# Optimization experiments

Hardware: AMD Instinct MI355X
Metric: run time of the kernel (lower is better)

Reference implementation:

```python
import jax, jax.numpy as jnp
import numpy as np

DIM = 2048
N_HEADS = 16
Q_LORA = 1536
KV_LORA = 512
NOPE = 128
ROPE = 64
QK_HD = NOPE + ROPE  # 192
V_HD = 128
BS, SEQ = 2, 2048
EPS = 1e-6


def rmsnorm(x, w):
    var = jnp.mean(jnp.square(x), axis=-1, keepdims=True)
    return x * jax.lax.rsqrt(var + EPS) * w


def rope_cos_sin(seq_len, dim, dtype):
    inv_freq = 1.0 / (10000.0 ** (jnp.arange(0, dim, 2, dtype=jnp.float32) / dim))
    t = jnp.arange(seq_len, dtype=jnp.float32)
    freqs = jnp.outer(t, inv_freq)            # [S, dim/2]
    emb = jnp.concatenate([freqs, freqs], -1)  # [S, dim]
    return jnp.cos(emb).astype(dtype), jnp.sin(emb).astype(dtype)


def rotate_half(x):
    x1, x2 = jnp.split(x, 2, axis=-1)
    return jnp.concatenate([-x2, x1], axis=-1)


def apply_rope(x, cos, sin):
    # x: [B, S, H, D]; cos/sin: [S, D] -> broadcast over B, H
    return x * cos[None, :, None, :] + rotate_half(x) * sin[None, :, None, :]


def setup_inputs() -> dict:
    key = jax.random.key(0)
    ks = jax.random.split(key, 8)
    s = 0.02
    return {
        "x": jax.random.normal(ks[0], (BS, SEQ, DIM), jnp.float32),
        "wq_a_w": jax.random.normal(ks[1], (Q_LORA, DIM), jnp.float32) * s,
        "wq_a_b": jnp.zeros((Q_LORA,), jnp.float32),
        "q_norm_w": jnp.ones((Q_LORA,), jnp.float32),
        "wq_b_w": jax.random.normal(ks[2], (N_HEADS * QK_HD, Q_LORA), jnp.float32) * s,
        "wq_b_b": jnp.zeros((N_HEADS * QK_HD,), jnp.float32),
        "wkv_a_w": jax.random.normal(ks[3], (KV_LORA + ROPE, DIM), jnp.float32) * s,
        "wkv_a_b": jnp.zeros((KV_LORA + ROPE,), jnp.float32),
        "kv_norm_w": jnp.ones((KV_LORA,), jnp.float32),
        "wkv_b_w": jax.random.normal(ks[4], (N_HEADS * (NOPE + V_HD), KV_LORA), jnp.float32) * s,
        "wkv_b_b": jnp.zeros((N_HEADS * (NOPE + V_HD),), jnp.float32),
        "wo_w": jax.random.normal(ks[5], (DIM, N_HEADS * V_HD), jnp.float32) * s,
        "wo_b": jnp.zeros((DIM,), jnp.float32),
    }


def reference(x, wq_a_w, wq_a_b, q_norm_w, wq_b_w, wq_b_b,
              wkv_a_w, wkv_a_b, kv_norm_w, wkv_b_w, wkv_b_b, wo_w, wo_b):
    bs, seq_len, _ = x.shape
    # Q path: low-rank down, RMSNorm, up
    q = x @ wq_a_w.T + wq_a_b
    q = rmsnorm(q, q_norm_w)
    q = q @ wq_b_w.T + wq_b_b
    q = q.reshape(bs, seq_len, N_HEADS, QK_HD)
    q_nope, q_pe = q[..., :NOPE], q[..., NOPE:]
    # KV path: joint low-rank + decoupled rope key
    kv = x @ wkv_a_w.T + wkv_a_b
    kv_c, k_pe = kv[..., :KV_LORA], kv[..., KV_LORA:]
    k_pe = k_pe[:, :, None, :]  # [B, S, 1, ROPE]
    cos, sin = rope_cos_sin(seq_len, ROPE, x.dtype)
    q_pe = apply_rope(q_pe, cos, sin)
    k_pe = apply_rope(k_pe, cos, sin)
    # naive mode: materialize per-head K/V
    kv_c = rmsnorm(kv_c, kv_norm_w)
    kvb = (kv_c @ wkv_b_w.T + wkv_b_b).reshape(bs, seq_len, N_HEADS, NOPE + V_HD)
    k_nope, v = kvb[..., :NOPE], kvb[..., NOPE:]
    q_full = jnp.concatenate([q_nope, q_pe], axis=-1)            # [B,S,H,192]
    k_full = jnp.concatenate(
        [k_nope, jnp.broadcast_to(k_pe, (bs, seq_len, N_HEADS, ROPE))], axis=-1)
    scale = 1.0 / np.sqrt(QK_HD)
    scores = jnp.einsum('bqhd,bkhd->bhqk', q_full, k_full) * scale
    causal = jnp.tril(jnp.ones((seq_len, seq_len), bool))
    scores = jnp.where(causal[None, None], scores, jnp.finfo(scores.dtype).min)
    attn = jax.nn.softmax(scores, axis=-1)
    out = jnp.einsum('bhqk,bkhd->bqhd', attn, v)
    out = out.reshape(bs, seq_len, N_HEADS * V_HD)
    return out @ wo_w.T + wo_b
```

## Files before the change

kernel.cpp:

```cpp
#include <hip/hip_runtime.h>

#define SEQ 2048
#define NHEADS 16

typedef __bf16 bf16;
typedef __bf16 bf16x8 __attribute__((ext_vector_type(8)));
typedef __bf16 bf16x4v __attribute__((ext_vector_type(4)));
typedef float f32x4 __attribute__((ext_vector_type(4)));

static __device__ __forceinline__ float bf2f(unsigned short u) {
    union { unsigned u32; float f; } v; v.u32 = ((unsigned)u) << 16; return v.f;
}
static __device__ __forceinline__ unsigned short f2bf(float f) {
    union { float f; unsigned u; } v; v.f = f;
    unsigned u = v.u;
    unsigned r = u + 0x7fffu + ((u >> 16) & 1u);
    return (unsigned short)(r >> 16);
}

static __device__ __forceinline__ void g2l16(const unsigned short* g, unsigned short* l) {
    __builtin_amdgcn_global_load_lds(
        (const __attribute__((address_space(1))) unsigned int*)(unsigned long long)g,
        (__attribute__((address_space(3))) unsigned int*)(unsigned int)(unsigned long long)l,
        16, 0, 0);
}

__global__ void detect_dtype(const unsigned* __restrict__ qnw, int* __restrict__ flag) {
    if (threadIdx.x == 0 && blockIdx.x == 0)
        *flag = (qnw[0] == 0x3F800000u) ? 1 : 0;
}

struct CvtArgs {
    const void* src[13];
    unsigned short* dst[13];
    int n[13];
    int startblk[14];
};
__global__ __launch_bounds__(256) void to_bf16_all(CvtArgs a, const int* __restrict__ flag) {
    int bx = blockIdx.x;
    int t = 0;
    while (bx >= a.startblk[t + 1]) ++t;
    int base = (bx - a.startblk[t]) * 4096;
    int n = a.n[t];
    int hi = base + 4096; if (hi > n) hi = n;
    if (*flag) {
        const float* s = (const float*)a.src[t];
        unsigned short* d = a.dst[t];
        for (int e = base + threadIdx.x; e < hi; e += 256) d[e] = f2bf(s[e]);
    } else {
        const unsigned short* s = (const unsigned short*)a.src[t];
        unsigned short* d = a.dst[t];
        for (int e = base + threadIdx.x; e < hi; e += 256) d[e] = s[e];
    }
}

__global__ __launch_bounds__(256) void gemm_bt_tile(
    const unsigned short* __restrict__ A, int lda,
    const unsigned short* __restrict__ W,
    const unsigned short* __restrict__ bias,
    unsigned short* __restrict__ C, float* __restrict__ Cf, int ldc,
    int N, int K, const int* __restrict__ flagp)
{
    __shared__ unsigned short Al[128 * 32];
    __shared__ unsigned short Bl[128 * 32];

    const int lane = threadIdx.x & 63;
    const int w    = threadIdx.x >> 6;
    const int r    = lane & 15;
    const int quad = lane >> 4;
    const int m0 = blockIdx.y << 7;
    const int n0 = blockIdx.x << 7;
    const int wr = (w >> 1) << 6;
    const int wc = (w & 1) << 6;

    const int srow = lane >> 2;
    const int scol = (lane & 3) << 3;
    const int j0 = w * 2, j1 = w * 2 + 1;

    const unsigned short* a0 = A + (size_t)(m0 + j0 * 16 + srow) * lda + scol;
    const unsigned short* a1 = A + (size_t)(m0 + j1 * 16 + srow) * lda + scol;
    int bn0 = n0 + j0 * 16 + srow; if (bn0 >= N) bn0 = N - 1;
    int bn1 = n0 + j1 * 16 + srow; if (bn1 >= N) bn1 = N - 1;
    const unsigned short* b0 = W + (size_t)bn0 * K + scol;
    const unsigned short* b1 = W + (size_t)bn1 * K + scol;

    f32x4 acc[4][4];
#pragma unroll
    for (int mt = 0; mt < 4; ++mt)
#pragma unroll
        for (int nt = 0; nt < 4; ++nt) acc[mt][nt] = (f32x4){0.f, 0.f, 0.f, 0.f};

    for (int kb = 0; kb < K; kb += 32) {
        __syncthreads();
        g2l16(a0 + kb, &Al[j0 * 512 + lane * 8]);
        g2l16(a1 + kb, &Al[j1 * 512 + lane * 8]);
        g2l16(b0 + kb, &Bl[j0 * 512 + lane * 8]);
        g2l16(b1 + kb, &Bl[j1 * 512 + lane * 8]);
        __syncthreads();

        bf16x8 af[4], bfr[4];
#pragma unroll
        for (int mt = 0; mt < 4; ++mt)
            af[mt] = *(const bf16x8*)&Al[(wr + mt * 16 + r) * 32 + quad * 8];
#pragma unroll
        for (int nt = 0; nt < 4; ++nt)
            bfr[nt] = *(const bf16x8*)&Bl[(wc + nt * 16 + r) * 32 + quad * 8];
#pragma unroll
        for (int mt = 0; mt < 4; ++mt)
#pragma unroll
            for (int nt = 0; nt < 4; ++nt)
                acc[mt][nt] = __builtin_amdgcn_mfma_f32_16x16x32_bf16(af[mt], bfr[nt], acc[mt][nt], 0, 0, 0);
    }

    int outf = (Cf && flagp) ? *flagp : 0;
    float bv[4];
#pragma unroll
    for (int nt = 0; nt < 4; ++nt) {
        int col = n0 + wc + nt * 16 + r;
        bv[nt] = (bias && col < N) ? bf2f(bias[col]) : 0.f;
    }
#pragma unroll
    for (int mt = 0; mt < 4; ++mt) {
#pragma unroll
        for (int i = 0; i < 4; ++i) {
            int row = m0 + wr + mt * 16 + quad * 4 + i;
#pragma unroll
            for (int nt = 0; nt < 4; ++nt) {
                int col = n0 + wc + nt * 16 + r;
                if (col < N) {
                    float v = acc[mt][nt][i] + bv[nt];
                    size_t idx = (size_t)row * ldc + col;
                    if (Cf) {
                        if (outf) Cf[idx] = v;
                        else      ((unsigned short*)Cf)[idx] = f2bf(v);
                    } else {
                        C[idx] = f2bf(v);
                    }
                }
            }
        }
    }
}

__global__ __launch_bounds__(256) void rmsnorm_ip(
    unsigned short* __restrict__ data, int stride, int width,
    const unsigned short* __restrict__ w)
{
    __shared__ float red[256];
    int row = blockIdx.x;
    unsigned short* p = data + (size_t)row * stride;
    float ss = 0.f;
    for (int j = threadIdx.x; j < width; j += 256) {
        float f = bf2f(p[j]);
        ss += f * f;
    }
    red[threadIdx.x] = ss;
    __syncthreads();
    for (int s = 128; s > 0; s >>= 1) {
        if ((int)threadIdx.x < s) red[threadIdx.x] += red[threadIdx.x + s];
        __syncthreads();
    }
    float rstd = rsqrtf(red[0] / (float)width + 1e-6f);
    for (int j = threadIdx.x; j < width; j += 256) {
        p[j] = f2bf(bf2f(p[j]) * rstd * bf2f(w[j]));
    }
}

__global__ void rope_ip(unsigned short* __restrict__ base, int rowstride,
                        int headstride, int nheads, int off)
{
    int row = blockIdx.x;
    int s = row & (SEQ - 1);
    int total = nheads * 32;
    for (int t = threadIdx.x; t < total; t += blockDim.x) {
        int h = t >> 5, i = t & 31;
        float inv = exp2f(-(float)i * (13.2877123795f / 32.0f));
        float ang = (float)s * inv;
        float c = cosf(ang), sn = sinf(ang);
        unsigned short* p = base + (size_t)row * rowstride + h * headstride + off;
        float x1 = bf2f(p[i]), x2 = bf2f(p[i + 32]);
        p[i]      = f2bf(x1 * c - x2 * sn);
        p[i + 32] = f2bf(x2 * c + x1 * sn);
    }
}

__global__ __launch_bounds__(256) void mla_attn_mfma(
    const unsigned short* __restrict__ qbuf,
    const unsigned short* __restrict__ kvb,
    const unsigned short* __restrict__ kvbuf,
    unsigned short* __restrict__ attn_out)
{
    __shared__ unsigned short Kt[2][32 * 200];
    __shared__ unsigned short Vt[2][128 * 40];
    __shared__ unsigned short Pm[4][16 * 40];

    const int bh = blockIdx.y;
    const int b = bh >> 4, h = bh & 15;
    const int tid  = threadIdx.x;
    const int lane = tid & 63;
    const int w    = tid >> 6;
    const int r    = lane & 15;
    const int quad = lane >> 4;
    const int rowk0 = b * SEQ;
    const float scale = 0.0721687836487f;

    int kldso[3];
    const unsigned short* ksrc[3];
    int krst[3];
#pragma unroll
    for (int j = 0; j < 3; ++j) {
        int v = tid + j * 256;
        int row = v / 24, c = v % 24;
        kldso[j] = row * 200 + c * 8;
        if (c < 16) { ksrc[j] = kvb + (size_t)(rowk0 + row) * 4096 + h * 256 + c * 8; krst[j] = 4096; }
        else        { ksrc[j] = kvbuf + (size_t)(rowk0 + row) * 576 + 512 + (c - 16) * 8; krst[j] = 576; }
    }
    const int vp  = tid & 15;
    const int vdc = tid >> 4;
    const unsigned short* vsrc = kvb + (size_t)(rowk0 + 2 * vp) * 4096 + h * 256 + 128 + vdc * 8;

    unsigned short* Pw = Pm[w];

#pragma unroll 1
    for (int half = 0; half < 2; ++half) {
        const int qt = half ? (31 - (int)blockIdx.x) : (int)blockIdx.x;
        const int qbase = qt * 64 + w * 16;
        const int nkb = 2 * qt + 2;
        const int itmax = 2 * qt + (w >> 1);

        bf16x8 qf[6];
        {
            const unsigned short* qp =
                qbuf + (size_t)(rowk0 + qbase + r) * 3072 + h * 192 + quad * 8;
#pragma unroll
            for (int t = 0; t < 6; ++t) {
                bf16x8 v = *(const bf16x8*)(qp + t * 32);
#pragma unroll
                for (int j = 0; j < 8; ++j) v[j] = (__bf16)((float)v[j] * scale);
                qf[t] = v;
            }
        }

        f32x4 O[8];
#pragma unroll
        for (int f = 0; f < 8; ++f) O[f] = (f32x4){0.f, 0.f, 0.f, 0.f};
        float mi = -1e30f, li = 0.f;

        uint4 pk0, pk1, pk2, pv0, pv1;

        __syncthreads();
        pk0 = *(const uint4*)(ksrc[0]);
        pk1 = *(const uint4*)(ksrc[1]);
        pk2 = *(const uint4*)(ksrc[2]);
        pv0 = *(const uint4*)(vsrc);
        pv1 = *(const uint4*)(vsrc + 4096);
        {
            *(uint4*)&Kt[0][kldso[0]] = pk0;
            *(uint4*)&Kt[0][kldso[1]] = pk1;
            *(uint4*)&Kt[0][kldso[2]] = pk2;
            const unsigned* ea = (const unsigned*)&pv0;
            const unsigned* eb = (const unsigned*)&pv1;
#pragma unroll
            for (int t = 0; t < 4; ++t) {
                unsigned pe = (ea[t] & 0xffffu) | (eb[t] << 16);
                unsigned po = (ea[t] >> 16) | (eb[t] & 0xffff0000u);
                *(unsigned*)&Vt[0][(vdc * 8 + 2 * t) * 40 + 2 * vp]     = pe;
                *(unsigned*)&Vt[0][(vdc * 8 + 2 * t + 1) * 40 + 2 * vp] = po;
            }
        }
        __syncthreads();

#pragma unroll 1
        for (int it = 0; it < nkb; ++it) {
            const int p = it & 1;
            const int kb = it * 32;
            const bool more = (it + 1 < nkb);

            if (more) {
                const size_t koff = (size_t)(kb + 32);
                pk0 = *(const uint4*)(ksrc[0] + koff * krst[0]);
                pk1 = *(const uint4*)(ksrc[1] + koff * krst[1]);
                pk2 = *(const uint4*)(ksrc[2] + koff * krst[2]);
                pv0 = *(const uint4*)(vsrc + koff * 4096);
                pv1 = *(const uint4*)(vsrc + koff * 4096 + 4096);
            }

            if (it <= itmax) {
                f32x4 s0 = {0.f, 0.f, 0.f, 0.f}, s1 = {0.f, 0.f, 0.f, 0.f};
#pragma unroll
                for (int t = 0; t < 6; ++t) {
                    bf16x8 k0 = *(const bf16x8*)&Kt[p][r * 200 + t * 32 + quad * 8];
                    bf16x8 k1 = *(const bf16x8*)&Kt[p][(16 + r) * 200 + t * 32 + quad * 8];
                    s0 = __builtin_amdgcn_mfma_f32_16x16x32_bf16(k0, qf[t], s0, 0, 0, 0);
                    s1 = __builtin_amdgcn_mfma_f32_16x16x32_bf16(k1, qf[t], s1, 0, 0, 0);
                }

                const int qrow = qbase + r;
                float a0[4], a1[4];
                float mx = -1e30f;
#pragma unroll
                for (int i = 0; i < 4; ++i) {
                    a0[i] = (kb + quad * 4 + i      <= qrow) ? s0[i] : -1e30f;
                    a1[i] = (kb + 16 + quad * 4 + i <= qrow) ? s1[i] : -1e30f;
                    mx = fmaxf(mx, fmaxf(a0[i], a1[i]));
                }
                mx = fmaxf(mx, __shfl_xor(mx, 16, 64));
                mx = fmaxf(mx, __shfl_xor(mx, 32, 64));
                float mn = fmaxf(mi, mx);
                float al = __expf(mi - mn);
                float p0[4], p1[4], ps = 0.f;
#pragma unroll
                for (int i = 0; i < 4; ++i) {
                    p0[i] = __expf(a0[i] - mn);
                    p1[i] = __expf(a1[i] - mn);
                    ps += p0[i] + p1[i];
                }
                ps += __shfl_xor(ps, 16, 64);
                ps += __shfl_xor(ps, 32, 64);
                li = li * al + ps;
                mi = mn;
                uint2 d0, d1;
                d0.x = (unsigned)f2bf(p0[0]) | ((unsigned)f2bf(p0[1]) << 16);
                d0.y = (unsigned)f2bf(p0[2]) | ((unsigned)f2bf(p0[3]) << 16);
                d1.x = (unsigned)f2bf(p1[0]) | ((unsigned)f2bf(p1[1]) << 16);
                d1.y = (unsigned)f2bf(p1[2]) | ((unsigned)f2bf(p1[3]) << 16);
                *(uint2*)&Pw[r * 40 + quad * 4]      = d0;
                *(uint2*)&Pw[r * 40 + 16 + quad * 4] = d1;
#pragma unroll
                for (int f = 0; f < 8; ++f) O[f] *= al;

                bf16x8 pf = *(const bf16x8*)&Pw[r * 40 + quad * 8];
#pragma unroll
                for (int f = 0; f < 8; ++f) {
                    bf16x8 vb = *(const bf16x8*)&Vt[p][(f * 16 + r) * 40 + quad * 8];
                    O[f] = __builtin_amdgcn_mfma_f32_16x16x32_bf16(vb, pf, O[f], 0, 0, 0);
                }
            }

            if (more) {
                const int q2 = 1 - p;
                *(uint4*)&Kt[q2][kldso[0]] = pk0;
                *(uint4*)&Kt[q2][kldso[1]] = pk1;
                *(uint4*)&Kt[q2][kldso[2]] = pk2;
                const unsigned* ea = (const unsigned*)&pv0;
                const unsigned* eb = (const unsigned*)&pv1;
#pragma unroll
                for (int t = 0; t < 4; ++t) {
                    unsigned pe = (ea[t] & 0xffffu) | (eb[t] << 16);
                    unsigned po = (ea[t] >> 16) | (eb[t] & 0xffff0000u);
                    *(unsigned*)&Vt[q2][(vdc * 8 + 2 * t) * 40 + 2 * vp]     = pe;
                    *(unsigned*)&Vt[q2][(vdc * 8 + 2 * t + 1) * 40 + 2 * vp] = po;
                }
                __syncthreads();
            }
        }

        float inv = (li > 0.f) ? (1.f / li) : 0.f;
        unsigned short* orow = attn_out + (size_t)(rowk0 + qbase + r) * 2048 + h * 128;
#pragma unroll
        for (int f = 0; f < 8; ++f) {
            bf16x4v o;
#pragma unroll
            for (int i = 0; i < 4; ++i) o[i] = (__bf16)(O[f][i] * inv);
            *(bf16x4v*)&orow[f * 16 + quad * 4] = o;
        }
    }
}

extern "C" void kernel_launch(void* const* d_in, const int* in_sizes, int n_in,
                              void* d_out, int out_size, void* d_ws, size_t ws_size,
                              hipStream_t stream)
{
    char* ws = (char*)d_ws;
    size_t off = 0;
    auto alloc = [&](size_t bytes) -> void* {
        void* p = ws + off;
        off = (off + bytes + 255) & ~(size_t)255;
        return p;
    };

    int* flag = (int*)alloc(256);

    const int nx = 4096 * 2048;
    unsigned short* xb    = (unsigned short*)alloc((size_t)nx * 2);
    unsigned short* wqa   = (unsigned short*)alloc((size_t)1536 * 2048 * 2);
    unsigned short* wqab  = (unsigned short*)alloc(1536 * 2);
    unsigned short* qnw   = (unsigned short*)alloc(1536 * 2);
    unsigned short* wqb   = (unsigned short*)alloc((size_t)3072 * 1536 * 2);
    unsigned short* wqbb  = (unsigned short*)alloc(3072 * 2);
    unsigned short* wkva  = (unsigned short*)alloc((size_t)576 * 2048 * 2);
    unsigned short* wkvab = (unsigned short*)alloc(576 * 2);
    unsigned short* kvnw  = (unsigned short*)alloc(512 * 2);
    unsigned short* wkvb  = (unsigned short*)alloc((size_t)4096 * 512 * 2);
    unsigned short* wkvbb = (unsigned short*)alloc(4096 * 2);
    unsigned short* wo    = (unsigned short*)alloc((size_t)2048 * 2048 * 2);
    unsigned short* wob   = (unsigned short*)alloc(2048 * 2);

    unsigned short* qa   = (unsigned short*)alloc((size_t)4096 * 1536 * 2);
    unsigned short* qbuf = (unsigned short*)alloc((size_t)4096 * 3072 * 2);
    unsigned short* kvbf = (unsigned short*)alloc((size_t)4096 * 576 * 2);
    unsigned short* kvb  = (unsigned short*)alloc((size_t)4096 * 4096 * 2);
    unsigned short* attn = xb;

    const int M = 4096;
    dim3 blk(256);

    detect_dtype<<<dim3(1), dim3(64), 0, stream>>>((const unsigned*)d_in[3], flag);

    {
        CvtArgs a;
        unsigned short* dsts[13] = {xb, wqa, wqab, qnw, wqb, wqbb, wkva, wkvab, kvnw, wkvb, wkvbb, wo, wob};
        int pb = 0;
        for (int i = 0; i < 13; ++i) {
            a.src[i] = d_in[i];
            a.dst[i] = dsts[i];
            a.n[i] = in_sizes[i];
            a.startblk[i] = pb;
            pb += (in_sizes[i] + 4095) / 4096;
        }
        a.startblk[13] = pb;
        to_bf16_all<<<dim3(pb), blk, 0, stream>>>(a, flag);
    }

    gemm_bt_tile<<<dim3(1536 / 128, M / 128), blk, 0, stream>>>(xb, 2048, wqa, wqab, qa, nullptr, 1536, 1536, 2048, nullptr);
    rmsnorm_ip<<<dim3(M), blk, 0, stream>>>(qa, 1536, 1536, qnw);
    gemm_bt_tile<<<dim3(3072 / 128, M / 128), blk, 0, stream>>>(qa, 1536, wqb, wqbb, qbuf, nullptr, 3072, 3072, 1536, nullptr);

    gemm_bt_tile<<<dim3((576 + 127) / 128, M / 128), blk, 0, stream>>>(xb, 2048, wkva, wkvab, kvbf, nullptr, 576, 576, 2048, nullptr);
    rmsnorm_ip<<<dim3(M), blk, 0, stream>>>(kvbf, 576, 512, kvnw);

    rope_ip<<<dim3(M), blk, 0, stream>>>(qbuf, 3072, 192, 16, 128);
    rope_ip<<<dim3(M), dim3(64), 0, stream>>>(kvbf, 576, 0, 1, 512);

    gemm_bt_tile<<<dim3(4096 / 128, M / 128), blk, 0, stream>>>(kvbf, 576, wkvb, wkvbb, kvb, nullptr, 4096, 4096, 512, nullptr);

    mla_attn_mfma<<<dim3(16, 2 * NHEADS), blk, 0, stream>>>(qbuf, kvb, kvbf, attn);

    gemm_bt_tile<<<dim3(2048 / 128, M / 128), blk, 0, stream>>>(attn, 2048, wo, wob, nullptr, (float*)d_out, 2048, 2048, 2048, flag);
}
```

Baseline: 539.2 us.

## Batch independent GEMMs and small kernels into shared launches, tune attention softmax

Groups independent GEMMs (q_a with kv_a, q_b with kv_b) into single grouped launches, merges the two RMSNorms into one launch and the two RoPE passes into one. This cuts launch count and fills the GPU better for small-N GEMMs. It also vectorises the bf16 conversion kernel. In attention it skips the causal mask on fully visible blocks, skips the online-softmax rescale unless the max grows by more than 8, and adds s_setprio around MFMA sections. RoPE now runs after the kv_b GEMM, which only reads the non-rope part of kvbf, so the ordering stays correct.

```diff
diff --git a/kernel.cpp b/kernel.cpp
--- a/kernel.cpp
+++ b/kernel.cpp
@@ -7,6 +7,7 @@
 typedef __bf16 bf16x8 __attribute__((ext_vector_type(8)));
 typedef __bf16 bf16x4v __attribute__((ext_vector_type(4)));
 typedef float f32x4 __attribute__((ext_vector_type(4)));
+typedef unsigned short u16x4 __attribute__((ext_vector_type(4)));
 
 static __device__ __forceinline__ float bf2f(unsigned short u) {
     union { unsigned u32; float f; } v; v.u32 = ((unsigned)u) << 16; return v.f;
@@ -43,33 +44,44 @@
     int base = (bx - a.startblk[t]) * 4096;
     int n = a.n[t];
     int hi = base + 4096; if (hi > n) hi = n;
+    int cnt = hi - base;
     if (*flag) {
-        const float* s = (const float*)a.src[t];
-        unsigned short* d = a.dst[t];
-        for (int e = base + threadIdx.x; e < hi; e += 256) d[e] = f2bf(s[e]);
+        const f32x4* s = (const f32x4*)a.src[t] + (base >> 2);
+        u16x4* d = (u16x4*)(a.dst[t] + base);
+        int c4 = cnt >> 2;
+        for (int e = threadIdx.x; e < c4; e += 256) {
+            f32x4 v = s[e];
+            u16x4 o;
+#pragma unroll
+            for (int j = 0; j < 4; ++j) o[j] = f2bf(v[j]);
+            d[e] = o;
+        }
     } else {
-        const unsigned short* s = (const unsigned short*)a.src[t];
-        unsigned short* d = a.dst[t];
-        for (int e = base + threadIdx.x; e < hi; e += 256) d[e] = s[e];
-    }
-}
-
-__global__ __launch_bounds__(256) void gemm_bt_tile(
-    const unsigned short* __restrict__ A, int lda,
-    const unsigned short* __restrict__ W,
-    const unsigned short* __restrict__ bias,
-    unsigned short* __restrict__ C, float* __restrict__ Cf, int ldc,
-    int N, int K, const int* __restrict__ flagp)
+        const uint4* s = (const uint4*)a.src[t] + (base >> 3);
+        uint4* d = (uint4*)(a.dst[t] + base);
+        int c8 = cnt >> 3;
+        for (int e = threadIdx.x; e < c8; e += 256) d[e] = s[e];
+    }
+}
+
+struct GemmP {
+    const unsigned short* A; int lda;
+    const unsigned short* W;
+    const unsigned short* bias;
+    unsigned short* C; float* Cf; int ldc;
+    int N; int K; const int* flagp;
+    int nbx;
+};
+
+static __device__ void gemm_body(const GemmP g, int bx, int by,
+                                 unsigned short* Al, unsigned short* Bl)
 {
-    __shared__ unsigned short Al[128 * 32];
-    __shared__ unsigned short Bl[128 * 32];
-
     const int lane = threadIdx.x & 63;
     const int w    = threadIdx.x >> 6;
     const int r    = lane & 15;
     const int quad = lane >> 4;
-    const int m0 = blockIdx.y << 7;
-    const int n0 = blockIdx.x << 7;
+    const int m0 = by << 7;
+    const int n0 = bx << 7;
     const int wr = (w >> 1) << 6;
     const int wc = (w & 1) << 6;
 
@@ -77,12 +89,12 @@
     const int scol = (lane & 3) << 3;
     const int j0 = w * 2, j1 = w * 2 + 1;
 
-    const unsigned short* a0 = A + (size_t)(m0 + j0 * 16 + srow) * lda + scol;
-    const unsigned short* a1 = A + (size_t)(m0 + j1 * 16 + srow) * lda + scol;
-    int bn0 = n0 + j0 * 16 + srow; if (bn0 >= N) bn0 = N - 1;
-    int bn1 = n0 + j1 * 16 + srow; if (bn1 >= N) bn1 = N - 1;
-    const unsigned short* b0 = W + (size_t)bn0 * K + scol;
-    const unsigned short* b1 = W + (size_t)bn1 * K + scol;
+    const unsigned short* a0 = g.A + (size_t)(m0 + j0 * 16 + srow) * g.lda + scol;
+    const unsigned short* a1 = g.A + (size_t)(m0 + j1 * 16 + srow) * g.lda + scol;
+    int bn0 = n0 + j0 * 16 + srow; if (bn0 >= g.N) bn0 = g.N - 1;
+    int bn1 = n0 + j1 * 16 + srow; if (bn1 >= g.N) bn1 = g.N - 1;
+    const unsigned short* b0 = g.W + (size_t)bn0 * g.K + scol;
+    const unsigned short* b1 = g.W + (size_t)bn1 * g.K + scol;
 
     f32x4 acc[4][4];
 #pragma unroll
@@ -90,7 +102,7 @@
 #pragma unroll
         for (int nt = 0; nt < 4; ++nt) acc[mt][nt] = (f32x4){0.f, 0.f, 0.f, 0.f};
 
-    for (int kb = 0; kb < K; kb += 32) {
+    for (int kb = 0; kb < g.K; kb += 32) {
         __syncthreads();
         g2l16(a0 + kb, &Al[j0 * 512 + lane * 8]);
         g2l16(a1 + kb, &Al[j1 * 512 + lane * 8]);
@@ -112,12 +124,12 @@
                 acc[mt][nt] = __builtin_amdgcn_mfma_f32_16x16x32_bf16(af[mt], bfr[nt], acc[mt][nt], 0, 0, 0);
     }
 
-    int outf = (Cf && flagp) ? *flagp : 0;
+    int outf = (g.Cf && g.flagp) ? *g.flagp : 0;
     float bv[4];
 #pragma unroll
     for (int nt = 0; nt < 4; ++nt) {
         int col = n0 + wc + nt * 16 + r;
-        bv[nt] = (bias && col < N) ? bf2f(bias[col]) : 0.f;
+        bv[nt] = (g.bias && col < g.N) ? bf2f(g.bias[col]) : 0.f;
     }
 #pragma unroll
     for (int mt = 0; mt < 4; ++mt) {
@@ -127,14 +139,14 @@
 #pragma unroll
             for (int nt = 0; nt < 4; ++nt) {
                 int col = n0 + wc + nt * 16 + r;
-                if (col < N) {
+                if (col < g.N) {
                     float v = acc[mt][nt][i] + bv[nt];
-                    size_t idx = (size_t)row * ldc + col;
-                    if (Cf) {
-                        if (outf) Cf[idx] = v;
-                        else      ((unsigned short*)Cf)[idx] = f2bf(v);
+                    size_t idx = (size_t)row * g.ldc + col;
+                    if (g.Cf) {
+                        if (outf) g.Cf[idx] = v;
+                        else      ((unsigned short*)g.Cf)[idx] = f2bf(v);
                     } else {
-                        C[idx] = f2bf(v);
+                        g.C[idx] = f2bf(v);
                     }
                 }
             }
@@ -142,13 +154,36 @@
     }
 }
 
-__global__ __launch_bounds__(256) void rmsnorm_ip(
-    unsigned short* __restrict__ data, int stride, int width,
-    const unsigned short* __restrict__ w)
+__global__ __launch_bounds__(256) void gemm_one(GemmP g) {
+    __shared__ unsigned short Al[128 * 32];
+    __shared__ unsigned short Bl[128 * 32];
+    gemm_body(g, blockIdx.x, blockIdx.y, Al, Bl);
+}
+
+__global__ __launch_bounds__(256) void gemm_two(GemmP g0, GemmP g1, int nblk0) {
+    __shared__ unsigned short Al[128 * 32];
+    __shared__ unsigned short Bl[128 * 32];
+    int id = blockIdx.x;
+    if (id < nblk0) {
+        gemm_body(g0, id % g0.nbx, id / g0.nbx, Al, Bl);
+    } else {
+        id -= nblk0;
+        gemm_body(g1, id % g1.nbx, id / g1.nbx, Al, Bl);
+    }
+}
+
+__global__ __launch_bounds__(256) void rmsnorm_ip2(
+    unsigned short* __restrict__ d0, int s0w, int w0w, const unsigned short* __restrict__ w0,
+    unsigned short* __restrict__ d1, int s1w, int w1w, const unsigned short* __restrict__ w1,
+    int rows0)
 {
     __shared__ float red[256];
     int row = blockIdx.x;
-    unsigned short* p = data + (size_t)row * stride;
+    unsigned short* p; const unsigned short* wt; int stride, width;
+    if (row < rows0) { p = d0; wt = w0; stride = s0w; width = w0w; }
+    else { row -= rows0; p = d1; wt = w1; stride = s1w; width = w1w; }
+    p += (size_t)row * stride;
+
     float ss = 0.f;
     for (int j = threadIdx.x; j < width; j += 256) {
         float f = bf2f(p[j]);
@@ -162,22 +197,23 @@
     }
     float rstd = rsqrtf(red[0] / (float)width + 1e-6f);
     for (int j = threadIdx.x; j < width; j += 256) {
-        p[j] = f2bf(bf2f(p[j]) * rstd * bf2f(w[j]));
-    }
-}
-
-__global__ void rope_ip(unsigned short* __restrict__ base, int rowstride,
-                        int headstride, int nheads, int off)
+        p[j] = f2bf(bf2f(p[j]) * rstd * bf2f(wt[j]));
+    }
+}
+
+__global__ __launch_bounds__(256) void rope_ip_all(
+    unsigned short* __restrict__ qbuf, unsigned short* __restrict__ kvbf)
 {
     int row = blockIdx.x;
     int s = row & (SEQ - 1);
-    int total = nheads * 32;
-    for (int t = threadIdx.x; t < total; t += blockDim.x) {
-        int h = t >> 5, i = t & 31;
+    for (int t = threadIdx.x; t < 544; t += 256) {
+        int i = t & 31;
         float inv = exp2f(-(float)i * (13.2877123795f / 32.0f));
         float ang = (float)s * inv;
         float c = cosf(ang), sn = sinf(ang);
-        unsigned short* p = base + (size_t)row * rowstride + h * headstride + off;
+        unsigned short* p;
+        if (t < 512) p = qbuf + (size_t)row * 3072 + (t >> 5) * 192 + 128;
+        else         p = kvbf + (size_t)row * 576 + 512;
         float x1 = bf2f(p[i]), x2 = bf2f(p[i + 32]);
         p[i]      = f2bf(x1 * c - x2 * sn);
         p[i + 32] = f2bf(x2 * c + x1 * sn);
@@ -287,6 +323,7 @@
 
             if (it <= itmax) {
                 f32x4 s0 = {0.f, 0.f, 0.f, 0.f}, s1 = {0.f, 0.f, 0.f, 0.f};
+                __builtin_amdgcn_s_setprio(1);
 #pragma unroll
                 for (int t = 0; t < 6; ++t) {
                     bf16x8 k0 = *(const bf16x8*)&Kt[p][r * 200 + t * 32 + quad * 8];
@@ -294,47 +331,66 @@
                     s0 = __builtin_amdgcn_mfma_f32_16x16x32_bf16(k0, qf[t], s0, 0, 0, 0);
                     s1 = __builtin_amdgcn_mfma_f32_16x16x32_bf16(k1, qf[t], s1, 0, 0, 0);
                 }
+                __builtin_amdgcn_s_setprio(0);
 
                 const int qrow = qbase + r;
                 float a0[4], a1[4];
                 float mx = -1e30f;
-#pragma unroll
-                for (int i = 0; i < 4; ++i) {
-                    a0[i] = (kb + quad * 4 + i      <= qrow) ? s0[i] : -1e30f;
-                    a1[i] = (kb + 16 + quad * 4 + i <= qrow) ? s1[i] : -1e30f;
-                    mx = fmaxf(mx, fmaxf(a0[i], a1[i]));
+                if (kb + 31 > qbase) {
+#pragma unroll
+                    for (int i = 0; i < 4; ++i) {
+                        a0[i] = (kb + quad * 4 + i      <= qrow) ? s0[i] : -1e30f;
+                        a1[i] = (kb + 16 + quad * 4 + i <= qrow) ? s1[i] : -1e30f;
+                        mx = fmaxf(mx, fmaxf(a0[i], a1[i]));
+                    }
+                } else {
+#pragma unroll
+                    for (int i = 0; i < 4; ++i) {
+                        a0[i] = s0[i];
+                        a1[i] = s1[i];
+                        mx = fmaxf(mx, fmaxf(a0[i], a1[i]));
+                    }
                 }
                 mx = fmaxf(mx, __shfl_xor(mx, 16, 64));
                 mx = fmaxf(mx, __shfl_xor(mx, 32, 64));
-                float mn = fmaxf(mi, mx);
-                float al = __expf(mi - mn);
+
+                if (!__all(mx <= mi + 8.f)) {
+                    float mn = fmaxf(mi, mx);
+                    float al = __expf(mi - mn);
+#pragma unroll
+                    for (int f = 0; f < 8; ++f) O[f] *= al;
+                    li *= al;
+                    mi = mn;
+                }
+
                 float p0[4], p1[4], ps = 0.f;
 #pragma unroll
                 for (int i = 0; i < 4; ++i) {
-                    p0[i] = __expf(a0[i] - mn);
-                    p1[i] = __expf(a1[i] - mn);
+                    p0[i] = __expf(a0[i] - mi);
+                    p1[i] = __expf(a1[i] - mi);
                     ps += p0[i] + p1[i];
                 }
                 ps += __shfl_xor(ps, 16, 64);
                 ps += __shfl_xor(ps, 32, 64);
-                li = li * al + ps;
-                mi = mn;
-                uint2 d0, d1;
-                d0.x = (unsigned)f2bf(p0[0]) | ((unsigned)f2bf(p0[1]) << 16);
-                d0.y = (unsigned)f2bf(p0[2]) | ((unsigned)f2bf(p0[3]) << 16);
-                d1.x = (unsigned)f2bf(p1[0]) | ((unsigned)f2bf(p1[1]) << 16);
-                d1.y = (unsigned)f2bf(p1[2]) | ((unsigned)f2bf(p1[3]) << 16);
-                *(uint2*)&Pw[r * 40 + quad * 4]      = d0;
-                *(uint2*)&Pw[r * 40 + 16 + quad * 4] = d1;
-#pragma unroll
-                for (int f = 0; f < 8; ++f) O[f] *= al;
+                li += ps;
+
+                bf16x4v b0v, b1v;
+#pragma unroll
+                for (int i = 0; i < 4; ++i) {
+                    b0v[i] = (__bf16)p0[i];
+                    b1v[i] = (__bf16)p1[i];
+                }
+                *(bf16x4v*)&Pw[r * 40 + quad * 4]      = b0v;
+                *(bf16x4v*)&Pw[r * 40 + 16 + quad * 4] = b1v;
 
                 bf16x8 pf = *(const bf16x8*)&Pw[r * 40 + quad * 8];
+                __builtin_amdgcn_s_setprio(1);
 #pragma unroll
                 for (int f = 0; f < 8; ++f) {
                     bf16x8 vb = *(const bf16x8*)&Vt[p][(f * 16 + r) * 40 + quad * 8];
                     O[f] = __builtin_amdgcn_mfma_f32_16x16x32_bf16(vb, pf, O[f], 0, 0, 0);
                 }
+                __builtin_amdgcn_s_setprio(0);
             }
 
             if (more) {
@@ -422,19 +478,39 @@
         to_bf16_all<<<dim3(pb), blk, 0, stream>>>(a, flag);
     }
 
-    gemm_bt_tile<<<dim3(1536 / 128, M / 128), blk, 0, stream>>>(xb, 2048, wqa, wqab, qa, nullptr, 1536, 1536, 2048, nullptr);
-    rmsnorm_ip<<<dim3(M), blk, 0, stream>>>(qa, 1536, 1536, qnw);
-    gemm_bt_tile<<<dim3(3072 / 128, M / 128), blk, 0, stream>>>(qa, 1536, wqb, wqbb, qbuf, nullptr, 3072, 3072, 1536, nullptr);
-
-    gemm_bt_tile<<<dim3((576 + 127) / 128, M / 128), blk, 0, stream>>>(xb, 2048, wkva, wkvab, kvbf, nullptr, 576, 576, 2048, nullptr);
-    rmsnorm_ip<<<dim3(M), blk, 0, stream>>>(kvbf, 576, 512, kvnw);
-
-    rope_ip<<<dim3(M), blk, 0, stream>>>(qbuf, 3072, 192, 16, 128);
-    rope_ip<<<dim3(M), dim3(64), 0, stream>>>(kvbf, 576, 0, 1, 512);
-
-    gemm_bt_tile<<<dim3(4096 / 128, M / 128), blk, 0, stream>>>(kvbf, 576, wkvb, wkvbb, kvb, nullptr, 4096, 4096, 512, nullptr);
+    auto mkg = [](const unsigned short* A, int lda, const unsigned short* W,
+                  const unsigned short* bias, unsigned short* C, float* Cf, int ldc,
+                  int N, int K, const int* fl) -> GemmP {
+        GemmP g;
+        g.A = A; g.lda = lda; g.W = W; g.bias = bias;
+        g.C = C; g.Cf = Cf; g.ldc = ldc; g.N = N; g.K = K; g.flagp = fl;
+        g.nbx = (N + 127) / 128;
+        return g;
+    };
+
+    {
+        GemmP gqa  = mkg(xb, 2048, wqa,  wqab,  qa,   nullptr, 1536, 1536, 2048, nullptr);
+        GemmP gkva = mkg(xb, 2048, wkva, wkvab, kvbf, nullptr, 576,  576,  2048, nullptr);
+        int nb0 = gqa.nbx * (M / 128), nb1 = gkva.nbx * (M / 128);
+        gemm_two<<<dim3(nb0 + nb1), blk, 0, stream>>>(gqa, gkva, nb0);
+    }
+
+    rmsnorm_ip2<<<dim3(2 * M), blk, 0, stream>>>(qa, 1536, 1536, qnw,
+                                                 kvbf, 576, 512, kvnw, M);
+
+    {
+        GemmP gqb  = mkg(qa,   1536, wqb,  wqbb,  qbuf, nullptr, 3072, 3072, 1536, nullptr);
+        GemmP gkvb = mkg(kvbf, 576,  wkvb, wkvbb, kvb,  nullptr, 4096, 4096, 512,  nullptr);
+        int nb0 = gqb.nbx * (M / 128), nb1 = gkvb.nbx * (M / 128);
+        gemm_two<<<dim3(nb0 + nb1), blk, 0, stream>>>(gqb, gkvb, nb0);
+    }
+
+    rope_ip_all<<<dim3(M), blk, 0, stream>>>(qbuf, kvbf);
 
     mla_attn_mfma<<<dim3(16, 2 * NHEADS), blk, 0, stream>>>(qbuf, kvb, kvbf, attn);
 
-    gemm_bt_tile<<<dim3(2048 / 128, M / 128), blk, 0, stream>>>(attn, 2048, wo, wob, nullptr, (float*)d_out, 2048, 2048, 2048, flag);
-}
+    {
+        GemmP gout = mkg(attn, 2048, wo, wob, nullptr, (float*)d_out, 2048, 2048, 2048, flag);
+        gemm_one<<<dim3(gout.nbx, M / 128), blk, 0, stream>>>(gout);
+    }
+}
```

Result: faster. 492.4 us (-8.7%).
